# Optimization experiments

Measured on AMD Instinct MI355X. Metric: run time of the kernel, lower is better.

## Reference

```python
import jax, jax.numpy as jnp
import numpy as np

N_NODES = 10000
N_EDGES = 320000
N_GRAPHS = 64
IN_DIM = 1
HID = 256


def setup_inputs() -> dict:
    key = jax.random.key(0)
    ks = jax.random.split(key, 12)
    s = 1.0 / np.sqrt(HID)
    inp = {
        "x": jax.random.normal(ks[0], (N_NODES, IN_DIM), dtype=jnp.float32),
        "edge_index": jax.random.randint(ks[1], (2, N_EDGES), 0, N_NODES, dtype=jnp.int64),
        "batch": jnp.sort(jax.random.randint(ks[2], (N_NODES,), 0, N_GRAPHS, dtype=jnp.int64)),
        "W_emb": jax.random.normal(ks[3], (IN_DIM, HID), dtype=jnp.float32),
        "b_emb": jnp.zeros((HID,), dtype=jnp.float32),
        "W1a": jax.random.normal(ks[4], (HID, HID), dtype=jnp.float32) * s,
        "b1a": jnp.zeros((HID,), dtype=jnp.float32),
        "W1b": jax.random.normal(ks[5], (HID, HID), dtype=jnp.float32) * s,
        "b1b": jnp.zeros((HID,), dtype=jnp.float32),
        "W2a": jax.random.normal(ks[6], (HID, HID), dtype=jnp.float32) * s,
        "b2a": jnp.zeros((HID,), dtype=jnp.float32),
        "W2b": jax.random.normal(ks[7], (HID, HID), dtype=jnp.float32) * s,
        "b2b": jnp.zeros((HID,), dtype=jnp.float32),
    }
    return inp


def _pointnet_conv(h, src, dst, Wa, ba, Wb, bb):
    # gather x_j -> 2-layer MLP per edge -> scatter-max at dst (PyG aggr='max')
    msg = jax.nn.relu(h[src] @ Wa + ba) @ Wb + bb          # [E, HID]
    agg = jax.ops.segment_max(msg, dst, num_segments=N_NODES)
    # PyG fills nodes with no incoming messages with 0
    return jnp.where(jnp.isneginf(agg), 0.0, agg)


def reference(x, edge_index, batch, W_emb, b_emb, W1a, b1a, W1b, b1b, W2a, b2a, W2b, b2b):
    src, dst = edge_index[0], edge_index[1]
    h = jax.nn.silu(x @ W_emb + b_emb)                     # [N, HID]
    h = h + jax.nn.silu(_pointnet_conv(h, src, dst, W1a, b1a, W1b, b1b))
    h = h + jax.nn.silu(_pointnet_conv(h, src, dst, W2a, b2a, W2b, b2b))
    # global_mean_pool over graphs
    sums = jax.ops.segment_sum(h, batch, num_segments=N_GRAPHS)          # [G, HID]
    cnts = jax.ops.segment_sum(jnp.ones((h.shape[0],), h.dtype), batch, num_segments=N_GRAPHS)
    return sums / jnp.maximum(cnts, 1.0)[:, None]
```

## Files before the change

### kernel.cpp

```cpp
#include <hip/hip_runtime.h>
#include <hip/hip_bf16.h>
#include <math.h>

#define HID 256
#define CAP 128
#define FB 64

typedef __attribute__((ext_vector_type(8))) short bf16x8;
typedef __attribute__((ext_vector_type(8))) unsigned short u16x8;
typedef __attribute__((ext_vector_type(4))) float f32x4;

__device__ __forceinline__ float silu_f(float z) {
    return z / (1.0f + __expf(-z));
}
__device__ __forceinline__ unsigned short f2bf(float f) {
    unsigned int u = __float_as_uint(f);
    u = (u + 0x7FFFu + ((u >> 16) & 1u)) >> 16;
    return (unsigned short)u;
}
__device__ __forceinline__ float bf2f(unsigned short b) {
    return __uint_as_float(((unsigned int)b) << 16);
}
__device__ __forceinline__ void max8(float m[8], u16x8 v) {
#pragma unroll
    for (int k = 0; k < 8; ++k) m[k] = fmaxf(m[k], bf2f(v[k]));
}

__global__ __launch_bounds__(256) void k_prep(
    const float* __restrict__ w0, const float* __restrict__ w1,
    const float* __restrict__ w2, const float* __restrict__ w3,
    unsigned short* __restrict__ o0, unsigned short* __restrict__ o1,
    unsigned short* __restrict__ o2, unsigned short* __restrict__ o3,
    const int* __restrict__ dst, int* __restrict__ cbase,
    const int* __restrict__ batch, int* __restrict__ goff,
    int N, int G, int E, int chunk) {
    __shared__ __align__(16) int shp[10000];
    int b = blockIdx.x;
    int tid = threadIdx.x;
    if (b < 64) {
        float (*ls)[65] = (float(*)[65])shp;
        int mat = b >> 4;
        int tile = b & 15;
        int k0 = (tile >> 2) * 64;
        int n0 = (tile & 3) * 64;
        const float* in = (mat == 0) ? w0 : (mat == 1) ? w1 : (mat == 2) ? w2 : w3;
        unsigned short* op = (mat == 0) ? o0 : (mat == 1) ? o1 : (mat == 2) ? o2 : o3;
        int lrb = tid >> 4;
        int lc = (tid & 15) * 4;
#pragma unroll
        for (int p = 0; p < 4; ++p) {
            int lr = p * 16 + lrb;
            float4 v = *(const float4*)(in + (size_t)(k0 + lr) * HID + n0 + lc);
            ls[lr][lc + 0] = v.x; ls[lr][lc + 1] = v.y;
            ls[lr][lc + 2] = v.z; ls[lr][lc + 3] = v.w;
        }
        __syncthreads();
#pragma unroll
        for (int p = 0; p < 4; ++p) {
            int ln = p * 16 + lrb;
            ushort4 q;
            q.x = f2bf(ls[lc + 0][ln]);
            q.y = f2bf(ls[lc + 1][ln]);
            q.z = f2bf(ls[lc + 2][ln]);
            q.w = f2bf(ls[lc + 3][ln]);
            *(ushort4*)(op + (size_t)(n0 + ln) * HID + k0 + lc) = q;
        }
    } else if (b == 64) {
        int g = tid;
        if (g > G) return;
        int lo = 0, hi = N;
        while (lo < hi) {
            int mid = (lo + hi) >> 1;
            if (batch[mid] < g) lo = mid + 1; else hi = mid;
        }
        goff[g] = lo;
    } else {
        int fb = b - 65;
        int* hist = shp;
        for (int i = tid; i < N; i += 256) hist[i] = 0;
        __syncthreads();
        int e0 = fb * chunk;
        int e1 = min(E, e0 + chunk);
        for (int e = e0 + tid * 4; e + 3 < e1; e += 1024) {
            int4 d4 = *(const int4*)(dst + e);
            atomicAdd(&hist[d4.x], 1);
            atomicAdd(&hist[d4.y], 1);
            atomicAdd(&hist[d4.z], 1);
            atomicAdd(&hist[d4.w], 1);
        }
        int rem = (e1 - e0) & 3;
        if (tid < rem) atomicAdd(&hist[dst[e1 - rem + tid]], 1);
        __syncthreads();
        for (int i = tid; i < N; i += 256) cbase[(size_t)fb * N + i] = hist[i];
    }
}

__global__ __launch_bounds__(256) void k_prefix(int* __restrict__ cbase,
                                                int* __restrict__ cnt, int N) {
    int d = blockIdx.x * 256 + threadIdx.x;
    if (d >= N) return;
    int run = 0;
#pragma unroll
    for (int b = 0; b < FB; ++b) {
        int c = cbase[(size_t)b * N + d];
        cbase[(size_t)b * N + d] = run;
        run += c;
    }
    cnt[d] = run;
}

__global__ __launch_bounds__(256) void k_mlp1f(
    const float* __restrict__ x, const float* __restrict__ Wemb,
    const float* __restrict__ bemb,
    const unsigned short* __restrict__ Wta, const float* __restrict__ ba,
    const unsigned short* __restrict__ Wtb, const float* __restrict__ bbv,
    unsigned short* __restrict__ hb, unsigned short* __restrict__ t2,
    const int* __restrict__ src, const int* __restrict__ dst,
    const int* __restrict__ cbase, unsigned short* __restrict__ csr,
    int M, int E, int MT, int chunk) {
    __shared__ __align__(16) int shbuf[10000];
    unsigned short (*As)[264]  = (unsigned short(*)[264])shbuf;
    unsigned short (*t1s)[264] = (unsigned short(*)[264])((char*)shbuf + 16896);
    int b = blockIdx.x;
    int tid = threadIdx.x;

    if (b >= MT) {
        int fb = b - MT;
        int* hist = shbuf;
        for (int i = tid; i < M; i += 256) hist[i] = 0;
        __syncthreads();
        int e0 = fb * chunk;
        int e1 = min(E, e0 + chunk);
        const int* cb = cbase + (size_t)fb * M;
        for (int e = e0 + tid * 4; e + 3 < e1; e += 1024) {
            int4 d4 = *(const int4*)(dst + e);
            int4 s4 = *(const int4*)(src + e);
            int r0 = atomicAdd(&hist[d4.x], 1);
            int r1 = atomicAdd(&hist[d4.y], 1);
            int r2 = atomicAdd(&hist[d4.z], 1);
            int r3 = atomicAdd(&hist[d4.w], 1);
            int p0 = cb[d4.x] + r0;
            int p1 = cb[d4.y] + r1;
            int p2 = cb[d4.z] + r2;
            int p3 = cb[d4.w] + r3;
            if (p0 < CAP) csr[d4.x * CAP + p0] = (unsigned short)s4.x;
            if (p1 < CAP) csr[d4.y * CAP + p1] = (unsigned short)s4.y;
            if (p2 < CAP) csr[d4.z * CAP + p2] = (unsigned short)s4.z;
            if (p3 < CAP) csr[d4.w * CAP + p3] = (unsigned short)s4.w;
        }
        int rem = (e1 - e0) & 3;
        if (tid < rem) {
            int e = e1 - rem + tid;
            int d = dst[e];
            int r = atomicAdd(&hist[d], 1);
            int p = cb[d] + r;
            if (p < CAP) csr[d * CAP + p] = (unsigned short)src[e];
        }
        return;
    }

    int lane = tid & 63;
    int wave = tid >> 6;
    int quad = lane >> 4;
    int r = lane & 15;
    int m0 = b * 32;
    int colw = wave * 64;

    {
        int row = tid >> 3;
        int c0 = (tid & 7) * 32;
        int grow = m0 + row;
        float xv = (grow < M) ? x[grow] : 0.0f;
#pragma unroll
        for (int j = 0; j < 8; ++j) {
            int c = c0 + j * 4;
            ushort4 q;
            q.x = f2bf(silu_f(xv * Wemb[c + 0] + bemb[c + 0]));
            q.y = f2bf(silu_f(xv * Wemb[c + 1] + bemb[c + 1]));
            q.z = f2bf(silu_f(xv * Wemb[c + 2] + bemb[c + 2]));
            q.w = f2bf(silu_f(xv * Wemb[c + 3] + bemb[c + 3]));
            if (grow < M) *(ushort4*)(hb + (size_t)grow * HID + c) = q;
            *(ushort4*)&As[row][c] = q;
        }
        __syncthreads();
    }

    f32x4 acc[2][4];
#pragma unroll
    for (int rt = 0; rt < 2; ++rt)
#pragma unroll
        for (int nt = 0; nt < 4; ++nt) acc[rt][nt] = (f32x4)0.0f;
#pragma unroll
    for (int ks = 0; ks < 8; ++ks) {
        bf16x8 a0 = *(const bf16x8*)&As[r][ks * 32 + quad * 8];
        bf16x8 a1 = *(const bf16x8*)&As[r + 16][ks * 32 + quad * 8];
#pragma unroll
        for (int nt = 0; nt < 4; ++nt) {
            bf16x8 bfr = *(const bf16x8*)(Wta + (size_t)(colw + nt * 16 + r) * HID
                                          + ks * 32 + quad * 8);
            acc[0][nt] = __builtin_amdgcn_mfma_f32_16x16x32_bf16(a0, bfr, acc[0][nt], 0, 0, 0);
            acc[1][nt] = __builtin_amdgcn_mfma_f32_16x16x32_bf16(a1, bfr, acc[1][nt], 0, 0, 0);
        }
    }
#pragma unroll
    for (int nt = 0; nt < 4; ++nt) {
        int col = colw + nt * 16 + r;
        float bv = ba[col];
#pragma unroll
        for (int rt = 0; rt < 2; ++rt)
#pragma unroll
            for (int i = 0; i < 4; ++i) {
                float v = fmaxf(acc[rt][nt][i] + bv, 0.0f);
                t1s[rt * 16 + quad * 4 + i][col] = f2bf(v);
            }
    }
    __syncthreads();

    f32x4 acc2[2][4];
#pragma unroll
    for (int rt = 0; rt < 2; ++rt)
#pragma unroll
        for (int nt = 0; nt < 4; ++nt) acc2[rt][nt] = (f32x4)0.0f;
#pragma unroll
    for (int ks = 0; ks < 8; ++ks) {
        bf16x8 a0 = *(const bf16x8*)&t1s[r][ks * 32 + quad * 8];
        bf16x8 a1 = *(const bf16x8*)&t1s[r + 16][ks * 32 + quad * 8];
#pragma unroll
        for (int nt = 0; nt < 4; ++nt) {
            bf16x8 bfr = *(const bf16x8*)(Wtb + (size_t)(colw + nt * 16 + r) * HID
                                          + ks * 32 + quad * 8);
            acc2[0][nt] = __builtin_amdgcn_mfma_f32_16x16x32_bf16(a0, bfr, acc2[0][nt], 0, 0, 0);
            acc2[1][nt] = __builtin_amdgcn_mfma_f32_16x16x32_bf16(a1, bfr, acc2[1][nt], 0, 0, 0);
        }
    }
#pragma unroll
    for (int nt = 0; nt < 4; ++nt) {
        int col = colw + nt * 16 + r;
        float bv = bbv[col];
#pragma unroll
        for (int rt = 0; rt < 2; ++rt)
#pragma unroll
            for (int i = 0; i < 4; ++i) {
                int row = m0 + rt * 16 + quad * 4 + i;
                if (row < M) t2[(size_t)row * HID + col] = f2bf(acc2[rt][nt][i] + bv);
            }
    }
}

__global__ __launch_bounds__(256) void k_mlp2(
    const unsigned short* __restrict__ Aglob,
    const unsigned short* __restrict__ Wta, const float* __restrict__ ba,
    const unsigned short* __restrict__ Wtb, const float* __restrict__ bbv,
    unsigned short* __restrict__ t2, int M) {
    __shared__ unsigned short t1s[32][264];
    int tid = threadIdx.x;
    int lane = tid & 63;
    int wave = tid >> 6;
    int quad = lane >> 4;
    int r = lane & 15;
    int m0 = blockIdx.x * 32;
    int colw = wave * 64;

    f32x4 acc[2][4];
#pragma unroll
    for (int rt = 0; rt < 2; ++rt)
#pragma unroll
        for (int nt = 0; nt < 4; ++nt) acc[rt][nt] = (f32x4)0.0f;

    int ar0 = m0 + r;        if (ar0 >= M) ar0 = M - 1;
    int ar1 = m0 + 16 + r;   if (ar1 >= M) ar1 = M - 1;

#pragma unroll
    for (int ks = 0; ks < 8; ++ks) {
        bf16x8 a0 = *(const bf16x8*)(Aglob + (size_t)ar0 * HID + ks * 32 + quad * 8);
        bf16x8 a1 = *(const bf16x8*)(Aglob + (size_t)ar1 * HID + ks * 32 + quad * 8);
#pragma unroll
        for (int nt = 0; nt < 4; ++nt) {
            bf16x8 bfr = *(const bf16x8*)(Wta + (size_t)(colw + nt * 16 + r) * HID
                                          + ks * 32 + quad * 8);
            acc[0][nt] = __builtin_amdgcn_mfma_f32_16x16x32_bf16(a0, bfr, acc[0][nt], 0, 0, 0);
            acc[1][nt] = __builtin_amdgcn_mfma_f32_16x16x32_bf16(a1, bfr, acc[1][nt], 0, 0, 0);
        }
    }
#pragma unroll
    for (int nt = 0; nt < 4; ++nt) {
        int col = colw + nt * 16 + r;
        float bv = ba[col];
#pragma unroll
        for (int rt = 0; rt < 2; ++rt)
#pragma unroll
            for (int i = 0; i < 4; ++i) {
                float v = fmaxf(acc[rt][nt][i] + bv, 0.0f);
                t1s[rt * 16 + quad * 4 + i][col] = f2bf(v);
            }
    }
    __syncthreads();

    f32x4 acc2[2][4];
#pragma unroll
    for (int rt = 0; rt < 2; ++rt)
#pragma unroll
        for (int nt = 0; nt < 4; ++nt) acc2[rt][nt] = (f32x4)0.0f;
#pragma unroll
    for (int ks = 0; ks < 8; ++ks) {
        bf16x8 a0 = *(const bf16x8*)&t1s[r][ks * 32 + quad * 8];
        bf16x8 a1 = *(const bf16x8*)&t1s[r + 16][ks * 32 + quad * 8];
#pragma unroll
        for (int nt = 0; nt < 4; ++nt) {
            bf16x8 bfr = *(const bf16x8*)(Wtb + (size_t)(colw + nt * 16 + r) * HID
                                          + ks * 32 + quad * 8);
            acc2[0][nt] = __builtin_amdgcn_mfma_f32_16x16x32_bf16(a0, bfr, acc2[0][nt], 0, 0, 0);
            acc2[1][nt] = __builtin_amdgcn_mfma_f32_16x16x32_bf16(a1, bfr, acc2[1][nt], 0, 0, 0);
        }
    }
#pragma unroll
    for (int nt = 0; nt < 4; ++nt) {
        int col = colw + nt * 16 + r;
        float bv = bbv[col];
#pragma unroll
        for (int rt = 0; rt < 2; ++rt)
#pragma unroll
            for (int i = 0; i < 4; ++i) {
                int row = m0 + rt * 16 + quad * 4 + i;
                if (row < M) t2[(size_t)row * HID + col] = f2bf(acc2[rt][nt][i] + bv);
            }
    }
}

__global__ __launch_bounds__(256) void k_agg(const unsigned short* __restrict__ t2,
                                             const int* __restrict__ cnt,
                                             const unsigned short* __restrict__ csr,
                                             unsigned short* __restrict__ hb, int N) {
    int lane = threadIdx.x & 63;
    int node = (blockIdx.x * blockDim.x + threadIdx.x) >> 6;
    if (node >= N) return;
    int half = lane >> 5;
    int lc = (lane & 31) * 8;
    const unsigned short* base = t2 + lc;

    int deg = cnt[node];
    if (deg > CAP) deg = CAP;
    const unsigned short* rowp = csr + (size_t)node * CAP;
    size_t o = (size_t)node * HID + lc;
    u16x8 hq = *(const u16x8*)(hb + o);

    float m[8];
#pragma unroll
    for (int k = 0; k < 8; ++k) m[k] = -INFINITY;

    int i = 0;
    for (; i + 16 <= deg; i += 16) {
        int s[8];
#pragma unroll
        for (int j = 0; j < 8; ++j) s[j] = rowp[i + 2 * j + half];
        u16x8 v[8];
#pragma unroll
        for (int j = 0; j < 8; ++j) v[j] = *(const u16x8*)(base + (size_t)s[j] * HID);
#pragma unroll
        for (int j = 0; j < 8; ++j) max8(m, v[j]);
    }
    if (i + 8 <= deg) {
        int s[4];
#pragma unroll
        for (int j = 0; j < 4; ++j) s[j] = rowp[i + 2 * j + half];
        u16x8 v[4];
#pragma unroll
        for (int j = 0; j < 4; ++j) v[j] = *(const u16x8*)(base + (size_t)s[j] * HID);
#pragma unroll
        for (int j = 0; j < 4; ++j) max8(m, v[j]);
        i += 8;
    }
    for (; i < deg; i += 2) {
        int idx = i + half; if (idx >= deg) idx = deg - 1;
        int s = rowp[idx];
        u16x8 v = *(const u16x8*)(base + (size_t)s * HID);
        max8(m, v);
    }

#pragma unroll
    for (int k = 0; k < 8; ++k) m[k] = fmaxf(m[k], __shfl_xor(m[k], 32, 64));
    if (deg == 0) {
#pragma unroll
        for (int k = 0; k < 8; ++k) m[k] = 0.0f;
    }

    if (half == 0) {
        u16x8 q;
#pragma unroll
        for (int k = 0; k < 8; ++k) q[k] = f2bf(bf2f(hq[k]) + silu_f(m[k]));
        *(u16x8*)(hb + o) = q;
    }
}

__global__ __launch_bounds__(1024) void k_pool(const unsigned short* __restrict__ hb,
                                               const int* __restrict__ goff,
                                               float* __restrict__ out) {
    __shared__ float part[3][HID];
    int g = blockIdx.x;
    int tid = threadIdx.x;
    int c = tid & 255;
    int chunk = tid >> 8;
    int beg = goff[g], end = goff[g + 1];
    float s = 0.f;
    for (int n = beg + chunk; n < end; n += 4) s += bf2f(hb[(size_t)n * HID + c]);
    if (chunk > 0) part[chunk - 1][c] = s;
    __syncthreads();
    if (chunk == 0) {
        s += part[0][c] + part[1][c] + part[2][c];
        int cnt = end - beg;
        out[g * HID + c] = s / (float)(cnt > 0 ? cnt : 1);
    }
}

extern "C" void kernel_launch(void* const* d_in, const int* in_sizes, int n_in,
                              void* d_out, int out_size, void* d_ws, size_t ws_size,
                              hipStream_t stream) {
    const float* x     = (const float*)d_in[0];
    const int*   ei    = (const int*)d_in[1];
    const int*   batch = (const int*)d_in[2];
    const float* Wemb  = (const float*)d_in[3];
    const float* bemb  = (const float*)d_in[4];
    const float* W1a   = (const float*)d_in[5];
    const float* b1a   = (const float*)d_in[6];
    const float* W1b   = (const float*)d_in[7];
    const float* b1b   = (const float*)d_in[8];
    const float* W2a   = (const float*)d_in[9];
    const float* b2a   = (const float*)d_in[10];
    const float* W2b   = (const float*)d_in[11];
    const float* b2b   = (const float*)d_in[12];
    float* out = (float*)d_out;

    const int N = in_sizes[0];
    const int E = in_sizes[1] / 2;
    const int G = out_size / HID;
    const int* src = ei;
    const int* dst = ei + E;

    char* ws = (char*)d_ws;
    unsigned short* hb   = (unsigned short*)ws; ws += (size_t)N * HID * 2;
    unsigned short* t2   = (unsigned short*)ws; ws += (size_t)N * HID * 2;
    unsigned short* Wt1a = (unsigned short*)ws; ws += (size_t)HID * HID * 2;
    unsigned short* Wt1b = (unsigned short*)ws; ws += (size_t)HID * HID * 2;
    unsigned short* Wt2a = (unsigned short*)ws; ws += (size_t)HID * HID * 2;
    unsigned short* Wt2b = (unsigned short*)ws; ws += (size_t)HID * HID * 2;
    int* cnt   = (int*)ws; ws += (size_t)N * 4;
    int* goff  = (int*)ws; ws += (size_t)(G + 1) * 4;
    int* cbase = (int*)ws; ws += (size_t)FB * N * 4;
    unsigned short* csr = (unsigned short*)ws; ws += (size_t)N * CAP * 2;

    const int chunk = (((E + FB - 1) / FB) + 3) & ~3;
    const int MT = (N + 31) / 32;

    k_prep<<<64 + 1 + FB, 256, 0, stream>>>(W1a, W1b, W2a, W2b,
                                            Wt1a, Wt1b, Wt2a, Wt2b,
                                            dst, cbase, batch, goff, N, G, E, chunk);

    k_prefix<<<(N + 255) / 256, 256, 0, stream>>>(cbase, cnt, N);

    k_mlp1f<<<MT + FB, 256, 0, stream>>>(x, Wemb, bemb, Wt1a, b1a, Wt1b, b1b,
                                         hb, t2, src, dst, cbase, csr, N, E, MT, chunk);

    int agg_blocks = (N * 64 + 255) / 256;

    k_agg<<<agg_blocks, 256, 0, stream>>>(t2, cnt, csr, hb, N);

    k_mlp2<<<MT, 256, 0, stream>>>(hb, Wt2a, b2a, Wt2b, b2b, t2, N);

    k_agg<<<agg_blocks, 256, 0, stream>>>(t2, cnt, csr, hb, N);

    k_pool<<<G, 1024, 0, stream>>>(hb, goff, out);
}
```

Measured before the change: 194.7 us.

## Pack histogram counters to 16 bits, double edge blocks, halve MLP row tile

The shared histogram now packs two 16-bit counters per word, halving LDS use, which allows the edge-bucketing block count to rise from 64 to 128. The MLP kernels now process 16 rows per block instead of 32, doubling the block count for more parallelism and occupancy at the cost of reloading weight fragments more often. The aggregation tail is replaced by a single clamped 8-wide gather that may issue redundant loads for low-degree remainders. The prefix pass now loops over twice as many chunks without unrolling.

```diff
diff --git a/kernel.cpp b/kernel.cpp
--- a/kernel.cpp
+++ b/kernel.cpp
@@ -4,7 +4,7 @@
 
 #define HID 256
 #define CAP 128
-#define FB 64
+#define FB 128
 
 typedef __attribute__((ext_vector_type(8))) short bf16x8;
 typedef __attribute__((ext_vector_type(8))) unsigned short u16x8;
@@ -34,7 +34,7 @@
     const int* __restrict__ dst, int* __restrict__ cbase,
     const int* __restrict__ batch, int* __restrict__ goff,
     int N, int G, int E, int chunk) {
-    __shared__ __align__(16) int shp[10000];
+    __shared__ __align__(16) unsigned int shp[5000];
     int b = blockIdx.x;
     int tid = threadIdx.x;
     if (b < 64) {
@@ -76,22 +76,27 @@
         goff[g] = lo;
     } else {
         int fb = b - 65;
-        int* hist = shp;
-        for (int i = tid; i < N; i += 256) hist[i] = 0;
+        unsigned int* hist = shp;
+        int N2 = (N + 1) >> 1;
+        for (int i = tid; i < N2; i += 256) hist[i] = 0u;
         __syncthreads();
         int e0 = fb * chunk;
         int e1 = min(E, e0 + chunk);
         for (int e = e0 + tid * 4; e + 3 < e1; e += 1024) {
             int4 d4 = *(const int4*)(dst + e);
-            atomicAdd(&hist[d4.x], 1);
-            atomicAdd(&hist[d4.y], 1);
-            atomicAdd(&hist[d4.z], 1);
-            atomicAdd(&hist[d4.w], 1);
+            atomicAdd(&hist[d4.x >> 1], 1u << ((d4.x & 1) * 16));
+            atomicAdd(&hist[d4.y >> 1], 1u << ((d4.y & 1) * 16));
+            atomicAdd(&hist[d4.z >> 1], 1u << ((d4.z & 1) * 16));
+            atomicAdd(&hist[d4.w >> 1], 1u << ((d4.w & 1) * 16));
         }
         int rem = (e1 - e0) & 3;
-        if (tid < rem) atomicAdd(&hist[dst[e1 - rem + tid]], 1);
+        if (tid < rem) {
+            int d = dst[e1 - rem + tid];
+            atomicAdd(&hist[d >> 1], 1u << ((d & 1) * 16));
+        }
         __syncthreads();
-        for (int i = tid; i < N; i += 256) cbase[(size_t)fb * N + i] = hist[i];
+        for (int i = tid; i < N; i += 256)
+            cbase[(size_t)fb * N + i] = (int)((hist[i >> 1] >> ((i & 1) * 16)) & 0xffffu);
     }
 }
 
@@ -100,7 +105,6 @@
     int d = blockIdx.x * 256 + threadIdx.x;
     if (d >= N) return;
     int run = 0;
-#pragma unroll
     for (int b = 0; b < FB; ++b) {
         int c = cbase[(size_t)b * N + d];
         cbase[(size_t)b * N + d] = run;
@@ -118,16 +122,17 @@
     const int* __restrict__ src, const int* __restrict__ dst,
     const int* __restrict__ cbase, unsigned short* __restrict__ csr,
     int M, int E, int MT, int chunk) {
-    __shared__ __align__(16) int shbuf[10000];
+    __shared__ __align__(16) unsigned int shbuf[5000];
     unsigned short (*As)[264]  = (unsigned short(*)[264])shbuf;
-    unsigned short (*t1s)[264] = (unsigned short(*)[264])((char*)shbuf + 16896);
+    unsigned short (*t1s)[264] = (unsigned short(*)[264])((char*)shbuf + 8448);
     int b = blockIdx.x;
     int tid = threadIdx.x;
 
     if (b >= MT) {
         int fb = b - MT;
-        int* hist = shbuf;
-        for (int i = tid; i < M; i += 256) hist[i] = 0;
+        unsigned int* hist = shbuf;
+        int N2 = (M + 1) >> 1;
+        for (int i = tid; i < N2; i += 256) hist[i] = 0u;
         __syncthreads();
         int e0 = fb * chunk;
         int e1 = min(E, e0 + chunk);
@@ -135,14 +140,14 @@
         for (int e = e0 + tid * 4; e + 3 < e1; e += 1024) {
             int4 d4 = *(const int4*)(dst + e);
             int4 s4 = *(const int4*)(src + e);
-            int r0 = atomicAdd(&hist[d4.x], 1);
-            int r1 = atomicAdd(&hist[d4.y], 1);
-            int r2 = atomicAdd(&hist[d4.z], 1);
-            int r3 = atomicAdd(&hist[d4.w], 1);
-            int p0 = cb[d4.x] + r0;
-            int p1 = cb[d4.y] + r1;
-            int p2 = cb[d4.z] + r2;
-            int p3 = cb[d4.w] + r3;
+            unsigned int o0 = atomicAdd(&hist[d4.x >> 1], 1u << ((d4.x & 1) * 16));
+            unsigned int o1 = atomicAdd(&hist[d4.y >> 1], 1u << ((d4.y & 1) * 16));
+            unsigned int o2 = atomicAdd(&hist[d4.z >> 1], 1u << ((d4.z & 1) * 16));
+            unsigned int o3 = atomicAdd(&hist[d4.w >> 1], 1u << ((d4.w & 1) * 16));
+            int p0 = cb[d4.x] + (int)((o0 >> ((d4.x & 1) * 16)) & 0xffffu);
+            int p1 = cb[d4.y] + (int)((o1 >> ((d4.y & 1) * 16)) & 0xffffu);
+            int p2 = cb[d4.z] + (int)((o2 >> ((d4.z & 1) * 16)) & 0xffffu);
+            int p3 = cb[d4.w] + (int)((o3 >> ((d4.w & 1) * 16)) & 0xffffu);
             if (p0 < CAP) csr[d4.x * CAP + p0] = (unsigned short)s4.x;
             if (p1 < CAP) csr[d4.y * CAP + p1] = (unsigned short)s4.y;
             if (p2 < CAP) csr[d4.z * CAP + p2] = (unsigned short)s4.z;
@@ -152,8 +157,8 @@
         if (tid < rem) {
             int e = e1 - rem + tid;
             int d = dst[e];
-            int r = atomicAdd(&hist[d], 1);
-            int p = cb[d] + r;
+            unsigned int o = atomicAdd(&hist[d >> 1], 1u << ((d & 1) * 16));
+            int p = cb[d] + (int)((o >> ((d & 1) * 16)) & 0xffffu);
             if (p < CAP) csr[d * CAP + p] = (unsigned short)src[e];
         }
         return;
@@ -163,16 +168,16 @@
     int wave = tid >> 6;
     int quad = lane >> 4;
     int r = lane & 15;
-    int m0 = b * 32;
+    int m0 = b * 16;
     int colw = wave * 64;
 
     {
-        int row = tid >> 3;
-        int c0 = (tid & 7) * 32;
+        int row = tid >> 4;
+        int c0 = (tid & 15) * 16;
         int grow = m0 + row;
         float xv = (grow < M) ? x[grow] : 0.0f;
 #pragma unroll
-        for (int j = 0; j < 8; ++j) {
+        for (int j = 0; j < 4; ++j) {
             int c = c0 + j * 4;
             ushort4 q;
             q.x = f2bf(silu_f(xv * Wemb[c + 0] + bemb[c + 0]));
@@ -185,21 +190,17 @@
         __syncthreads();
     }
 
-    f32x4 acc[2][4];
-#pragma unroll
-    for (int rt = 0; rt < 2; ++rt)
-#pragma unroll
-        for (int nt = 0; nt < 4; ++nt) acc[rt][nt] = (f32x4)0.0f;
+    f32x4 acc[4];
+#pragma unroll
+    for (int nt = 0; nt < 4; ++nt) acc[nt] = (f32x4)0.0f;
 #pragma unroll
     for (int ks = 0; ks < 8; ++ks) {
         bf16x8 a0 = *(const bf16x8*)&As[r][ks * 32 + quad * 8];
-        bf16x8 a1 = *(const bf16x8*)&As[r + 16][ks * 32 + quad * 8];
 #pragma unroll
         for (int nt = 0; nt < 4; ++nt) {
             bf16x8 bfr = *(const bf16x8*)(Wta + (size_t)(colw + nt * 16 + r) * HID
                                           + ks * 32 + quad * 8);
-            acc[0][nt] = __builtin_amdgcn_mfma_f32_16x16x32_bf16(a0, bfr, acc[0][nt], 0, 0, 0);
-            acc[1][nt] = __builtin_amdgcn_mfma_f32_16x16x32_bf16(a1, bfr, acc[1][nt], 0, 0, 0);
+            acc[nt] = __builtin_amdgcn_mfma_f32_16x16x32_bf16(a0, bfr, acc[nt], 0, 0, 0);
         }
     }
 #pragma unroll
@@ -207,30 +208,24 @@
         int col = colw + nt * 16 + r;
         float bv = ba[col];
 #pragma unroll
-        for (int rt = 0; rt < 2; ++rt)
-#pragma unroll
-            for (int i = 0; i < 4; ++i) {
-                float v = fmaxf(acc[rt][nt][i] + bv, 0.0f);
-                t1s[rt * 16 + quad * 4 + i][col] = f2bf(v);
-            }
+        for (int i = 0; i < 4; ++i) {
+            float v = fmaxf(acc[nt][i] + bv, 0.0f);
+            t1s[quad * 4 + i][col] = f2bf(v);
+        }
     }
     __syncthreads();
 
-    f32x4 acc2[2][4];
-#pragma unroll
-    for (int rt = 0; rt < 2; ++rt)
-#pragma unroll
-        for (int nt = 0; nt < 4; ++nt) acc2[rt][nt] = (f32x4)0.0f;
+    f32x4 acc2[4];
+#pragma unroll
+    for (int nt = 0; nt < 4; ++nt) acc2[nt] = (f32x4)0.0f;
 #pragma unroll
     for (int ks = 0; ks < 8; ++ks) {
         bf16x8 a0 = *(const bf16x8*)&t1s[r][ks * 32 + quad * 8];
-        bf16x8 a1 = *(const bf16x8*)&t1s[r + 16][ks * 32 + quad * 8];
 #pragma unroll
         for (int nt = 0; nt < 4; ++nt) {
             bf16x8 bfr = *(const bf16x8*)(Wtb + (size_t)(colw + nt * 16 + r) * HID
                                           + ks * 32 + quad * 8);
-            acc2[0][nt] = __builtin_amdgcn_mfma_f32_16x16x32_bf16(a0, bfr, acc2[0][nt], 0, 0, 0);
-            acc2[1][nt] = __builtin_amdgcn_mfma_f32_16x16x32_bf16(a1, bfr, acc2[1][nt], 0, 0, 0);
+            acc2[nt] = __builtin_amdgcn_mfma_f32_16x16x32_bf16(a0, bfr, acc2[nt], 0, 0, 0);
         }
     }
 #pragma unroll
@@ -238,12 +233,10 @@
         int col = colw + nt * 16 + r;
         float bv = bbv[col];
 #pragma unroll
-        for (int rt = 0; rt < 2; ++rt)
-#pragma unroll
-            for (int i = 0; i < 4; ++i) {
-                int row = m0 + rt * 16 + quad * 4 + i;
-                if (row < M) t2[(size_t)row * HID + col] = f2bf(acc2[rt][nt][i] + bv);
-            }
+        for (int i = 0; i < 4; ++i) {
+            int row = m0 + quad * 4 + i;
+            if (row < M) t2[(size_t)row * HID + col] = f2bf(acc2[nt][i] + bv);
+        }
     }
 }
 
@@ -252,34 +245,29 @@
     const unsigned short* __restrict__ Wta, const float* __restrict__ ba,
     const unsigned short* __restrict__ Wtb, const float* __restrict__ bbv,
     unsigned short* __restrict__ t2, int M) {
-    __shared__ unsigned short t1s[32][264];
+    __shared__ unsigned short t1s[16][264];
     int tid = threadIdx.x;
     int lane = tid & 63;
     int wave = tid >> 6;
     int quad = lane >> 4;
     int r = lane & 15;
-    int m0 = blockIdx.x * 32;
+    int m0 = blockIdx.x * 16;
     int colw = wave * 64;
 
-    f32x4 acc[2][4];
-#pragma unroll
-    for (int rt = 0; rt < 2; ++rt)
-#pragma unroll
-        for (int nt = 0; nt < 4; ++nt) acc[rt][nt] = (f32x4)0.0f;
+    f32x4 acc[4];
+#pragma unroll
+    for (int nt = 0; nt < 4; ++nt) acc[nt] = (f32x4)0.0f;
 
     int ar0 = m0 + r;        if (ar0 >= M) ar0 = M - 1;
-    int ar1 = m0 + 16 + r;   if (ar1 >= M) ar1 = M - 1;
 
 #pragma unroll
     for (int ks = 0; ks < 8; ++ks) {
         bf16x8 a0 = *(const bf16x8*)(Aglob + (size_t)ar0 * HID + ks * 32 + quad * 8);
-        bf16x8 a1 = *(const bf16x8*)(Aglob + (size_t)ar1 * HID + ks * 32 + quad * 8);
 #pragma unroll
         for (int nt = 0; nt < 4; ++nt) {
             bf16x8 bfr = *(const bf16x8*)(Wta + (size_t)(colw + nt * 16 + r) * HID
                                           + ks * 32 + quad * 8);
-            acc[0][nt] = __builtin_amdgcn_mfma_f32_16x16x32_bf16(a0, bfr, acc[0][nt], 0, 0, 0);
-            acc[1][nt] = __builtin_amdgcn_mfma_f32_16x16x32_bf16(a1, bfr, acc[1][nt], 0, 0, 0);
+            acc[nt] = __builtin_amdgcn_mfma_f32_16x16x32_bf16(a0, bfr, acc[nt], 0, 0, 0);
         }
     }
 #pragma unroll
@@ -287,30 +275,24 @@
         int col = colw + nt * 16 + r;
         float bv = ba[col];
 #pragma unroll
-        for (int rt = 0; rt < 2; ++rt)
-#pragma unroll
-            for (int i = 0; i < 4; ++i) {
-                float v = fmaxf(acc[rt][nt][i] + bv, 0.0f);
-                t1s[rt * 16 + quad * 4 + i][col] = f2bf(v);
-            }
+        for (int i = 0; i < 4; ++i) {
+            float v = fmaxf(acc[nt][i] + bv, 0.0f);
+            t1s[quad * 4 + i][col] = f2bf(v);
+        }
     }
     __syncthreads();
 
-    f32x4 acc2[2][4];
-#pragma unroll
-    for (int rt = 0; rt < 2; ++rt)
-#pragma unroll
-        for (int nt = 0; nt < 4; ++nt) acc2[rt][nt] = (f32x4)0.0f;
+    f32x4 acc2[4];
+#pragma unroll
+    for (int nt = 0; nt < 4; ++nt) acc2[nt] = (f32x4)0.0f;
 #pragma unroll
     for (int ks = 0; ks < 8; ++ks) {
         bf16x8 a0 = *(const bf16x8*)&t1s[r][ks * 32 + quad * 8];
-        bf16x8 a1 = *(const bf16x8*)&t1s[r + 16][ks * 32 + quad * 8];
 #pragma unroll
         for (int nt = 0; nt < 4; ++nt) {
             bf16x8 bfr = *(const bf16x8*)(Wtb + (size_t)(colw + nt * 16 + r) * HID
                                           + ks * 32 + quad * 8);
-            acc2[0][nt] = __builtin_amdgcn_mfma_f32_16x16x32_bf16(a0, bfr, acc2[0][nt], 0, 0, 0);
-            acc2[1][nt] = __builtin_amdgcn_mfma_f32_16x16x32_bf16(a1, bfr, acc2[1][nt], 0, 0, 0);
+            acc2[nt] = __builtin_amdgcn_mfma_f32_16x16x32_bf16(a0, bfr, acc2[nt], 0, 0, 0);
         }
     }
 #pragma unroll
@@ -318,12 +300,10 @@
         int col = colw + nt * 16 + r;
         float bv = bbv[col];
 #pragma unroll
-        for (int rt = 0; rt < 2; ++rt)
-#pragma unroll
-            for (int i = 0; i < 4; ++i) {
-                int row = m0 + rt * 16 + quad * 4 + i;
-                if (row < M) t2[(size_t)row * HID + col] = f2bf(acc2[rt][nt][i] + bv);
-            }
+        for (int i = 0; i < 4; ++i) {
+            int row = m0 + quad * 4 + i;
+            if (row < M) t2[(size_t)row * HID + col] = f2bf(acc2[nt][i] + bv);
+        }
     }
 }
 
@@ -359,22 +339,18 @@
 #pragma unroll
         for (int j = 0; j < 8; ++j) max8(m, v[j]);
     }
-    if (i + 8 <= deg) {
-        int s[4];
-#pragma unroll
-        for (int j = 0; j < 4; ++j) s[j] = rowp[i + 2 * j + half];
-        u16x8 v[4];
-#pragma unroll
-        for (int j = 0; j < 4; ++j) v[j] = *(const u16x8*)(base + (size_t)s[j] * HID);
-#pragma unroll
-        for (int j = 0; j < 4; ++j) max8(m, v[j]);
-        i += 8;
-    }
-    for (; i < deg; i += 2) {
-        int idx = i + half; if (idx >= deg) idx = deg - 1;
-        int s = rowp[idx];
-        u16x8 v = *(const u16x8*)(base + (size_t)s * HID);
-        max8(m, v);
+    if (i < deg) {
+        int s[8];
+#pragma unroll
+        for (int j = 0; j < 8; ++j) {
+            int idx = i + 2 * j + half; if (idx >= deg) idx = deg - 1;
+            s[j] = rowp[idx];
+        }
+        u16x8 v[8];
+#pragma unroll
+        for (int j = 0; j < 8; ++j) v[j] = *(const u16x8*)(base + (size_t)s[j] * HID);
+#pragma unroll
+        for (int j = 0; j < 8; ++j) max8(m, v[j]);
     }
 
 #pragma unroll
@@ -449,7 +425,7 @@
     unsigned short* csr = (unsigned short*)ws; ws += (size_t)N * CAP * 2;
 
     const int chunk = (((E + FB - 1) / FB) + 3) & ~3;
-    const int MT = (N + 31) / 32;
+    const int MT = (N + 15) / 16;
 
     k_prep<<<64 + 1 + FB, 256, 0, stream>>>(W1a, W1b, W2a, W2b,
                                             Wt1a, Wt1b, Wt2a, Wt2b,
```

Measured after the change: 209.8 us. 7.7% more time.
